# Kernel optimization log

Measured on AMD Instinct MI355X. Metric: run time of the kernel, lower is better.

Reference implementation:

```python
import jax, jax.numpy as jnp
import numpy as np

EPS = 1e-6


def softmax_kernel_transformation(data, is_query, projection_matrix):
    # data: [B,L,H,D], projection_matrix: [M,D]
    d = data.shape[-1]
    m = projection_matrix.shape[0]
    data_normalizer = 1.0 / jnp.sqrt(jnp.sqrt(jnp.float32(d)))
    data = data_normalizer * data
    ratio = 1.0 / jnp.sqrt(jnp.float32(m))
    data_dash = jnp.einsum('blhd,md->blhm', data, projection_matrix)
    diag_data = jnp.sum(jnp.square(data), axis=-1, keepdims=True) / 2.0  # [B,L,H,1]
    if is_query:
        stab = jnp.max(data_dash, axis=-1, keepdims=True)  # per-position max over M
    else:
        stab = jnp.max(data_dash, axis=(1, 3), keepdims=True)  # max over L and M
    return ratio * (jnp.exp(data_dash - diag_data - stab) + EPS)


def causal_linear_attention(qp, kp, v):
    # qp,kp: [L,B,H,M]; v: [L,B,H,D]. Sequential prefix-sum recurrence (FAVOR+ causal).
    B, H, M = qp.shape[1], qp.shape[2], qp.shape[3]
    D = v.shape[-1]
    kv0 = jnp.zeros((B, H, M, D), dtype=v.dtype)
    ks0 = jnp.zeros((B, H, M), dtype=kp.dtype)

    def step(carry, inp):
        kv_sum, k_sum = carry
        q_t, k_t, v_t = inp  # [B,H,M], [B,H,M], [B,H,D]
        kv_sum = kv_sum + jnp.einsum('bhm,bhd->bhmd', k_t, v_t)
        k_sum = k_sum + k_t
        num_t = jnp.einsum('bhmd,bhm->bhd', kv_sum, q_t)  # numerator row
        den_t = jnp.einsum('bhm,bhm->bh', q_t, k_sum)     # normalizer row
        return (kv_sum, k_sum), (num_t, den_t)

    (_, _), (num, den) = jax.lax.scan(step, (kv0, ks0), (qp, kp, v))
    return num, den  # [L,B,H,D], [L,B,H]


def favor_attention(query, key, value, projection_matrix):
    query_prime = softmax_kernel_transformation(query, True, projection_matrix)   # [B,L,H,M]
    key_prime = softmax_kernel_transformation(key, False, projection_matrix)      # [B,L,H,M]
    qp = jnp.transpose(query_prime, (1, 0, 2, 3))  # [L,B,H,M]
    kp = jnp.transpose(key_prime, (1, 0, 2, 3))
    v = jnp.transpose(value, (1, 0, 2, 3))         # [L,B,H,D]
    num, den = causal_linear_attention(qp, kp, v)
    av = jnp.transpose(num, (1, 0, 2, 3))          # [B,L,H,D]
    norm = jnp.transpose(den, (1, 0, 2))[..., None]  # [B,L,H,1]
    return av / norm


def setup_inputs() -> dict:
    B, L, H, D, M = 2, 2048, 8, 64, 128
    root = jax.random.key(0)
    kq, kk, kv, kp = jax.random.split(root, 4)
    return {
        'query': jax.random.normal(kq, (B, L, H, D), dtype=jnp.float32),
        'key': jax.random.normal(kk, (B, L, H, D), dtype=jnp.float32),
        'value': jax.random.normal(kv, (B, L, H, D), dtype=jnp.float32),
        'projection_matrix': jax.random.normal(kp, (M, D), dtype=jnp.float32),
    }


def reference(query, key, value, projection_matrix):
    return favor_attention(query, key, value, projection_matrix)
```

## Files before the change

kernel.cpp:

```cpp
#include <hip/hip_runtime.h>
#include <math.h>

typedef __attribute__((ext_vector_type(8))) short short8;
typedef __attribute__((ext_vector_type(4))) float f32x4;
typedef __attribute__((ext_vector_type(4))) unsigned short u16x4;

constexpr int B_ = 2, L_ = 2048, H_ = 8, D_ = 64, M_ = 128;
constexpr int T_ = 64;
constexpr int C_ = L_ / T_;
constexpr float DN_ = 0.35355339059327373f;
constexpr float RATIO_ = 0.08838834764831845f;
constexpr float EPSV_ = 1e-6f;
constexpr float REPS_ = RATIO_ * EPSV_;
constexpr float KEPS_ = 64.0f * REPS_;

__device__ inline unsigned short f2bf(float x) {
  const unsigned u = __float_as_uint(x);
  return (unsigned short)((u + 0x7fffu + ((u >> 16) & 1u)) >> 16);
}
__device__ inline float bf2f(unsigned short h) {
  return __uint_as_float(((unsigned)h) << 16);
}

__global__ __launch_bounds__(256) void psplit_kernel(
    const float* __restrict__ P, unsigned short* __restrict__ Ph,
    unsigned short* __restrict__ Pl) {
  const int i = blockIdx.x * 256 + threadIdx.x;
  const f32x4 t4 = *reinterpret_cast<const f32x4*>(&P[(size_t)i * 4]);
  u16x4 hi, lo;
#pragma unroll
  for (int j = 0; j < 4; ++j) {
    hi[j] = f2bf(t4[j]);
    lo[j] = f2bf(t4[j] - bf2f(hi[j]));
  }
  *reinterpret_cast<u16x4*>(&Ph[(size_t)i * 4]) = hi;
  *reinterpret_cast<u16x4*>(&Pl[(size_t)i * 4]) = lo;
}

__global__ __launch_bounds__(256) void feat_kernel(
    const float* __restrict__ q, const float* __restrict__ k,
    const unsigned short* __restrict__ Ph, const unsigned short* __restrict__ Pl,
    const float* __restrict__ v, unsigned short* __restrict__ qp16,
    unsigned short* __restrict__ kp16, unsigned short* __restrict__ kvc16,
    float* __restrict__ ksc, unsigned short* __restrict__ vt16,
    float* __restrict__ blockmax, float* __restrict__ vsum) {
  __shared__ __align__(16) unsigned short sm[27648];
  __shared__ float diag_s[T_];
  __shared__ float wred_s[2][T_];
  __shared__ float red4_s[4];

  const int sub = blockIdx.x;
  const int c = sub % C_, bh = sub / C_;
  const int b = bh >> 3, h = bh & 7;
  const int tid = threadIdx.x;
  const int w = tid >> 6, lane = tid & 63;
  const int l15 = lane & 15, l16 = lane >> 4;
  const int rblk = (w >> 1) * 32, cblk = (w & 1) * 64;

  for (int i8 = tid; i8 < M_ * 8; i8 += 256) {
    const int m = i8 >> 3, d0 = (i8 & 7) * 8;
    *reinterpret_cast<short8*>(&sm[9216 + m * 72 + d0]) =
        *reinterpret_cast<const short8*>(&Ph[m * D_ + d0]);
    *reinterpret_cast<short8*>(&sm[18432 + m * 72 + d0]) =
        *reinterpret_cast<const short8*>(&Pl[m * D_ + d0]);
  }

#define STAGE_X(xptr)                                                         \
  for (int i4 = tid; i4 < T_ * 16; i4 += 256) {                               \
    const int r = i4 >> 4, d0 = (i4 & 15) * 4;                                \
    f32x4 t4 = *reinterpret_cast<const f32x4*>(                               \
        &(xptr)[((size_t)(b * L_ + c * T_ + r) * H_ + h) * D_ + d0]);         \
    u16x4 hi, lo;                                                             \
    float sq = 0.f;                                                           \
    _Pragma("unroll") for (int j = 0; j < 4; ++j) {                           \
      const float xv = t4[j] * DN_;                                           \
      sq += xv * xv;                                                          \
      const unsigned short hb = f2bf(xv);                                     \
      hi[j] = hb;                                                             \
      lo[j] = f2bf(xv - bf2f(hb));                                            \
    }                                                                         \
    *reinterpret_cast<u16x4*>(&sm[r * 72 + d0]) = hi;                         \
    *reinterpret_cast<u16x4*>(&sm[4608 + r * 72 + d0]) = lo;                  \
    _Pragma("unroll") for (int off = 1; off < 16; off <<= 1)                  \
        sq += __shfl_xor(sq, off, 64);                                        \
    if ((tid & 15) == 0) diag_s[r] = sq;                                      \
  }

#define DASH_MFMA(accv)                                                       \
  _Pragma("unroll") for (int kk = 0; kk < 2; ++kk) {                          \
    short8 ah[2], al[2], bh8[4], bl8[4];                                      \
    _Pragma("unroll") for (int ti = 0; ti < 2; ++ti) {                        \
      ah[ti] = *reinterpret_cast<const short8*>(                              \
          &sm[(rblk + ti * 16 + l15) * 72 + kk * 32 + l16 * 8]);              \
      al[ti] = *reinterpret_cast<const short8*>(                              \
          &sm[4608 + (rblk + ti * 16 + l15) * 72 + kk * 32 + l16 * 8]);       \
    }                                                                         \
    _Pragma("unroll") for (int tj = 0; tj < 4; ++tj) {                        \
      bh8[tj] = *reinterpret_cast<const short8*>(                             \
          &sm[9216 + (cblk + tj * 16 + l15) * 72 + kk * 32 + l16 * 8]);       \
      bl8[tj] = *reinterpret_cast<const short8*>(                             \
          &sm[18432 + (cblk + tj * 16 + l15) * 72 + kk * 32 + l16 * 8]);      \
    }                                                                         \
    _Pragma("unroll") for (int ti = 0; ti < 2; ++ti)                          \
        _Pragma("unroll") for (int tj = 0; tj < 4; ++tj) {                    \
      accv[ti][tj] = __builtin_amdgcn_mfma_f32_16x16x32_bf16(                 \
          al[ti], bh8[tj], accv[ti][tj], 0, 0, 0);                            \
      accv[ti][tj] = __builtin_amdgcn_mfma_f32_16x16x32_bf16(                 \
          ah[ti], bl8[tj], accv[ti][tj], 0, 0, 0);                            \
      accv[ti][tj] = __builtin_amdgcn_mfma_f32_16x16x32_bf16(                 \
          ah[ti], bh8[tj], accv[ti][tj], 0, 0, 0);                            \
    }                                                                         \
  }

  STAGE_X(q);
  __syncthreads();
  f32x4 acc[2][4];
#pragma unroll
  for (int i = 0; i < 2; ++i)
#pragma unroll
    for (int j = 0; j < 4; ++j) acc[i][j] = {0.f, 0.f, 0.f, 0.f};
  DASH_MFMA(acc);

  {
    float rmax[2][4];
#pragma unroll
    for (int ti = 0; ti < 2; ++ti)
#pragma unroll
      for (int j = 0; j < 4; ++j) {
        float m0 = fmaxf(fmaxf(acc[ti][0][j], acc[ti][1][j]),
                         fmaxf(acc[ti][2][j], acc[ti][3][j]));
#pragma unroll
        for (int off = 1; off < 16; off <<= 1)
          m0 = fmaxf(m0, __shfl_xor(m0, off, 64));
        rmax[ti][j] = m0;
      }
    if (l15 == 0) {
#pragma unroll
      for (int ti = 0; ti < 2; ++ti)
#pragma unroll
        for (int j = 0; j < 4; ++j)
          wred_s[w & 1][rblk + ti * 16 + l16 * 4 + j] = rmax[ti][j];
    }
    __syncthreads();
#pragma unroll
    for (int ti = 0; ti < 2; ++ti)
#pragma unroll
      for (int j = 0; j < 4; ++j) {
        const int row = rblk + ti * 16 + l16 * 4 + j;
        const float sub2 =
            0.5f * diag_s[row] + fmaxf(wred_s[0][row], wred_s[1][row]);
#pragma unroll
        for (int tj = 0; tj < 4; ++tj) {
          const int col = cblk + tj * 16 + l15;
          sm[row * 136 + col] =
              f2bf(RATIO_ * (expf(acc[ti][tj][j] - sub2) + EPSV_));
        }
      }
    __syncthreads();
    unsigned short* outr = qp16 + ((size_t)bh * L_ + c * T_) * M_;
    for (int i8 = tid; i8 < T_ * 16; i8 += 256) {
      const int row = i8 >> 4, m0 = (i8 & 15) * 8;
      *reinterpret_cast<short8*>(&outr[row * M_ + m0]) =
          *reinterpret_cast<const short8*>(&sm[row * 136 + m0]);
    }
  }
  __syncthreads();

  STAGE_X(k);
  __syncthreads();
#pragma unroll
  for (int i = 0; i < 2; ++i)
#pragma unroll
    for (int j = 0; j < 4; ++j) acc[i][j] = {0.f, 0.f, 0.f, 0.f};
  DASH_MFMA(acc);

  float bm = -INFINITY;
#pragma unroll
  for (int ti = 0; ti < 2; ++ti)
#pragma unroll
    for (int tj = 0; tj < 4; ++tj)
#pragma unroll
      for (int j = 0; j < 4; ++j) bm = fmaxf(bm, acc[ti][tj][j]);
#pragma unroll
  for (int off = 1; off < 64; off <<= 1) bm = fmaxf(bm, __shfl_xor(bm, off, 64));
  if (lane == 0) red4_s[w] = bm;
  __syncthreads();
  const float lmax =
      fmaxf(fmaxf(red4_s[0], red4_s[1]), fmaxf(red4_s[2], red4_s[3]));
  if (tid == 0) blockmax[sub] = lmax;

  unsigned short* kpr = kp16 + ((size_t)bh * L_ + c * T_) * M_;
#pragma unroll
  for (int ti = 0; ti < 2; ++ti)
#pragma unroll
    for (int j = 0; j < 4; ++j) {
      const int row = rblk + ti * 16 + l16 * 4 + j;
      const float sub2 = 0.5f * diag_s[row] + lmax;
#pragma unroll
      for (int tj = 0; tj < 4; ++tj) {
        const int col = cblk + tj * 16 + l15;
        const unsigned short us = f2bf(RATIO_ * expf(acc[ti][tj][j] - sub2));
        kpr[row * M_ + col] = us;
        sm[9216 + col * 72 + row] = us;
      }
    }
  for (int i = tid; i < T_ * D_; i += 256) {
    const int t = i & 63, d = i >> 6;
    sm[d * 72 + t] =
        f2bf(v[((size_t)(b * L_ + c * T_ + t) * H_ + h) * D_ + d]);
  }
  __syncthreads();

  unsigned short* vg = vt16 + (size_t)(bh * C_ + c) * (D_ * T_);
  for (int i8 = tid; i8 < D_ * 8; i8 += 256) {
    const int d = i8 >> 3, t0 = (i8 & 7) * 8;
    *reinterpret_cast<short8*>(&vg[d * T_ + t0]) =
        *reinterpret_cast<const short8*>(&sm[d * 72 + t0]);
  }
  if (tid < M_) {
    float s = 0.f;
#pragma unroll
    for (int t8 = 0; t8 < 8; ++t8) {
      const short8 h8 =
          *reinterpret_cast<const short8*>(&sm[9216 + tid * 72 + t8 * 8]);
#pragma unroll
      for (int j = 0; j < 8; ++j) s += bf2f((unsigned short)h8[j]);
    }
    ksc[(size_t)(bh * C_ + c) * M_ + tid] = s;
  }
  if (tid >= 128 && tid < 128 + D_) {
    const int d = tid - 128;
    float s = 0.f;
#pragma unroll
    for (int t8 = 0; t8 < 8; ++t8) {
      const short8 h8 = *reinterpret_cast<const short8*>(&sm[d * 72 + t8 * 8]);
#pragma unroll
      for (int j = 0; j < 8; ++j) s += bf2f((unsigned short)h8[j]);
    }
    vsum[(size_t)(bh * C_ + c) * D_ + d] = s;
  }
  f32x4 acc2[2][4];
#pragma unroll
  for (int i = 0; i < 2; ++i)
#pragma unroll
    for (int j = 0; j < 4; ++j) acc2[i][j] = {0.f, 0.f, 0.f, 0.f};
#pragma unroll
  for (int kk = 0; kk < 2; ++kk) {
    short8 av[2], bv[4];
#pragma unroll
    for (int ti = 0; ti < 2; ++ti)
      av[ti] = *reinterpret_cast<const short8*>(
          &sm[(rblk + ti * 16 + l15) * 72 + kk * 32 + l16 * 8]);
#pragma unroll
    for (int tj = 0; tj < 4; ++tj)
      bv[tj] = *reinterpret_cast<const short8*>(
          &sm[9216 + (cblk + tj * 16 + l15) * 72 + kk * 32 + l16 * 8]);
#pragma unroll
    for (int ti = 0; ti < 2; ++ti)
#pragma unroll
      for (int tj = 0; tj < 4; ++tj)
        acc2[ti][tj] = __builtin_amdgcn_mfma_f32_16x16x32_bf16(
            av[ti], bv[tj], acc2[ti][tj], 0, 0, 0);
  }
#pragma unroll
  for (int ti = 0; ti < 2; ++ti)
#pragma unroll
    for (int j = 0; j < 4; ++j) {
      const int row = rblk + ti * 16 + l16 * 4 + j;
#pragma unroll
      for (int tj = 0; tj < 4; ++tj) {
        const int col = cblk + tj * 16 + l15;
        sm[18432 + row * 136 + col] = f2bf(acc2[ti][tj][j]);
      }
    }
  __syncthreads();
  unsigned short* ob = kvc16 + (size_t)(bh * C_ + c) * (M_ * D_);
  for (int i8 = tid; i8 < D_ * 16; i8 += 256) {
    const int d = i8 >> 4, m0 = (i8 & 15) * 8;
    *reinterpret_cast<short8*>(&ob[d * M_ + m0]) =
        *reinterpret_cast<const short8*>(&sm[18432 + d * 136 + m0]);
  }
#undef STAGE_X
#undef DASH_MFMA
}

__global__ __launch_bounds__(256) void prefix_kernel(
    const unsigned short* __restrict__ kvc16,
    unsigned short* __restrict__ kvp16, float* __restrict__ ksc,
    const float* __restrict__ blockmax, const float* __restrict__ vsum) {
  __shared__ float bm_s[C_];
  __shared__ float sc_s[C_];
  __shared__ float vs_s[2][C_];
  const int bid = blockIdx.x;
  const int ej = bid & 31, bh = bid >> 5;
  if (threadIdx.x < C_) bm_s[threadIdx.x] = blockmax[bh * C_ + threadIdx.x];
  if (threadIdx.x >= 64 && threadIdx.x < 64 + 2 * C_) {
    const int t = threadIdx.x - 64;
    const int ld = t >> 5, cc = t & 31;
    vs_s[ld][cc] = vsum[(size_t)(bh * C_ + cc) * D_ + ej * 2 + ld];
  }
  __syncthreads();
  if (threadIdx.x < C_) {
    float km = -INFINITY;
#pragma unroll
    for (int cc = 0; cc < C_; ++cc) km = fmaxf(km, bm_s[cc]);
    sc_s[threadIdx.x] = expf(bm_s[threadIdx.x] - km);
  }
  __syncthreads();
  const int e = ej * 256 + threadIdx.x;
  const int dl = threadIdx.x >> 7;
  float vals[C_];
#pragma unroll
  for (int cc = 0; cc < C_; ++cc)
    vals[cc] = bf2f(kvc16[(size_t)(bh * C_ + cc) * (M_ * D_) + e]) * sc_s[cc] +
               REPS_ * vs_s[dl][cc];
  float run = 0.f;
#pragma unroll
  for (int cc = 0; cc < C_; ++cc) {
    const float t = vals[cc];
    vals[cc] = run;
    run += t;
  }
#pragma unroll
  for (int cc = 0; cc < C_; ++cc)
    kvp16[(size_t)(bh * C_ + cc) * (M_ * D_) + e] = f2bf(vals[cc]);
  if (ej == 0 && threadIdx.x < M_) {
    const int m = threadIdx.x;
    float ks[C_];
#pragma unroll
    for (int cc = 0; cc < C_; ++cc)
      ks[cc] = ksc[(size_t)(bh * C_ + cc) * M_ + m] * sc_s[cc] + KEPS_;
    float rs = 0.f;
#pragma unroll
    for (int cc = 0; cc < C_; ++cc) {
      const float t = ks[cc];
      ks[cc] = rs;
      rs += t;
    }
#pragma unroll
    for (int cc = 0; cc < C_; ++cc)
      ksc[(size_t)(bh * C_ + cc) * M_ + m] = ks[cc];
  }
}

__global__ __launch_bounds__(256, 3) void intra_kernel(
    const unsigned short* __restrict__ qp16,
    const unsigned short* __restrict__ kp16,
    const unsigned short* __restrict__ vt16,
    const unsigned short* __restrict__ kvp16, const float* __restrict__ ksp,
    const float* __restrict__ blockmax, float* __restrict__ out) {
  __shared__ __align__(16) unsigned short qp_s[T_][136];
  __shared__ __align__(16) unsigned short kp_s[T_][136];
  __shared__ __align__(16) unsigned short S_s[T_][72];
  __shared__ float ksp_s[M_];
  __shared__ float denp_s[4][T_];
  __shared__ float den_s[T_];
  __shared__ float qsum_s[T_];
  __shared__ float bm_s[C_];

  const int bid = blockIdx.x;
  const int c = bid % C_, bh = bid / C_;
  const int b = bh >> 3, h = bh & 7;
  const int tid = threadIdx.x;
  const int w = tid >> 6, lane = tid & 63;
  const int l15 = lane & 15, l16 = lane >> 4;

  const unsigned short* qpt = qp16 + ((size_t)bh * L_ + c * T_) * M_;
  const unsigned short* kpt = kp16 + ((size_t)bh * L_ + c * T_) * M_;
  const unsigned short* kvt = kvp16 + (size_t)(bh * C_ + c) * (M_ * D_);
  const unsigned short* vg = vt16 + (size_t)(bh * C_ + c) * (D_ * T_);

  if (tid < C_) bm_s[tid] = blockmax[bh * C_ + tid];
  for (int i8 = tid; i8 < T_ * 16; i8 += 256) {
    const int r = i8 >> 4, m0 = (i8 & 15) * 8;
    *reinterpret_cast<short8*>(&qp_s[r][m0]) =
        *reinterpret_cast<const short8*>(&qpt[r * M_ + m0]);
    *reinterpret_cast<short8*>(&kp_s[r][m0]) =
        *reinterpret_cast<const short8*>(&kpt[r * M_ + m0]);
  }
  if (tid < M_) ksp_s[tid] = ksp[(size_t)(bh * C_ + c) * M_ + tid];
  __syncthreads();

  {
    const int row = w * 16 + (lane >> 2), mseg = (lane & 3) * 32;
    float p = 0.f;
#pragma unroll
    for (int u = 0; u < 4; ++u) {
      const short8 h8 =
          *reinterpret_cast<const short8*>(&qp_s[row][mseg + u * 8]);
#pragma unroll
      for (int j = 0; j < 8; ++j) p += bf2f((unsigned short)h8[j]);
    }
    p += __shfl_xor(p, 1, 64);
    p += __shfl_xor(p, 2, 64);
    if ((lane & 3) == 0) qsum_s[row] = p;
  }
  __syncthreads();

  float km = -INFINITY;
#pragma unroll
  for (int cc = 0; cc < C_; ++cc) km = fmaxf(km, bm_s[cc]);
  const float sc = expf(bm_s[c] - km);

  const int rblk = (w >> 1) * 32, cblk = (w & 1) * 32;
  f32x4 Sacc[2][2];
#pragma unroll
  for (int i = 0; i < 2; ++i)
#pragma unroll
    for (int j = 0; j < 2; ++j) Sacc[i][j] = {0.f, 0.f, 0.f, 0.f};

#pragma unroll
  for (int kk = 0; kk < 4; ++kk) {
    short8 af[2], bf[2];
#pragma unroll
    for (int ti = 0; ti < 2; ++ti)
      af[ti] = *reinterpret_cast<const short8*>(
          &qp_s[rblk + ti * 16 + l15][kk * 32 + l16 * 8]);
#pragma unroll
    for (int tj = 0; tj < 2; ++tj)
      bf[tj] = *reinterpret_cast<const short8*>(
          &kp_s[cblk + tj * 16 + l15][kk * 32 + l16 * 8]);
#pragma unroll
    for (int ti = 0; ti < 2; ++ti)
#pragma unroll
      for (int tj = 0; tj < 2; ++tj)
        Sacc[ti][tj] = __builtin_amdgcn_mfma_f32_16x16x32_bf16(
            af[ti], bf[tj], Sacc[ti][tj], 0, 0, 0);
  }
#pragma unroll
  for (int ti = 0; ti < 2; ++ti)
#pragma unroll
    for (int tj = 0; tj < 2; ++tj)
#pragma unroll
      for (int j = 0; j < 4; ++j) {
        const int row = rblk + ti * 16 + l16 * 4 + j;
        const int col = cblk + tj * 16 + l15;
        const float add = REPS_ * qsum_s[row];
        const float sv = (col <= row) ? Sacc[ti][tj][j] * sc + add : 0.f;
        S_s[row][col] = f2bf(sv);
      }
  __syncthreads();

  {
    const int t = lane;
    float p = 0.f;
    if (w == 0) {
      for (int tp = 0; tp < 32; ++tp) p += bf2f(S_s[t][tp]);
    } else if (w == 1) {
      for (int tp = 32; tp < 64; ++tp) p += bf2f(S_s[t][tp]);
    } else if (w == 2) {
      for (int m = 0; m < 64; ++m) p += bf2f(qp_s[t][m]) * ksp_s[m];
    } else {
      for (int m = 64; m < 128; ++m) p += bf2f(qp_s[t][m]) * ksp_s[m];
    }
    denp_s[w][t] = p;
  }
  __syncthreads();
  if (tid < T_)
    den_s[tid] =
        denp_s[0][tid] + denp_s[1][tid] + denp_s[2][tid] + denp_s[3][tid];
  __syncthreads();

  const int dblk = (w & 1) * 32;
  f32x4 Nacc[2][2];
#pragma unroll
  for (int i = 0; i < 2; ++i)
#pragma unroll
    for (int j = 0; j < 2; ++j) Nacc[i][j] = {0.f, 0.f, 0.f, 0.f};

#pragma unroll
  for (int kk = 0; kk < 2; ++kk) {
    short8 af[2], bf[2];
#pragma unroll
    for (int ti = 0; ti < 2; ++ti)
      af[ti] = *reinterpret_cast<const short8*>(
          &S_s[rblk + ti * 16 + l15][kk * 32 + l16 * 8]);
#pragma unroll
    for (int tj = 0; tj < 2; ++tj)
      bf[tj] = *reinterpret_cast<const short8*>(
          &vg[(dblk + tj * 16 + l15) * T_ + kk * 32 + l16 * 8]);
#pragma unroll
    for (int ti = 0; ti < 2; ++ti)
#pragma unroll
      for (int tj = 0; tj < 2; ++tj)
        Nacc[ti][tj] = __builtin_amdgcn_mfma_f32_16x16x32_bf16(
            af[ti], bf[tj], Nacc[ti][tj], 0, 0, 0);
  }
#pragma unroll
  for (int kk = 0; kk < 4; ++kk) {
    short8 af[2], bf[2];
#pragma unroll
    for (int ti = 0; ti < 2; ++ti)
      af[ti] = *reinterpret_cast<const short8*>(
          &qp_s[rblk + ti * 16 + l15][kk * 32 + l16 * 8]);
#pragma unroll
    for (int tj = 0; tj < 2; ++tj)
      bf[tj] = *reinterpret_cast<const short8*>(
          &kvt[(dblk + tj * 16 + l15) * M_ + kk * 32 + l16 * 8]);
#pragma unroll
    for (int ti = 0; ti < 2; ++ti)
#pragma unroll
      for (int tj = 0; tj < 2; ++tj)
        Nacc[ti][tj] = __builtin_amdgcn_mfma_f32_16x16x32_bf16(
            af[ti], bf[tj], Nacc[ti][tj], 0, 0, 0);
  }

#pragma unroll
  for (int ti = 0; ti < 2; ++ti)
#pragma unroll
    for (int j = 0; j < 4; ++j) {
      const int row = rblk + ti * 16 + l16 * 4 + j;
      const float r = 1.f / den_s[row];
      float* orow = out + ((size_t)(b * L_ + c * T_ + row) * H_ + h) * D_;
#pragma unroll
      for (int tj = 0; tj < 2; ++tj) {
        const int col = dblk + tj * 16 + l15;
        orow[col] = Nacc[ti][tj][j] * r;
      }
    }
}

extern "C" void kernel_launch(void* const* d_in, const int* in_sizes, int n_in,
                              void* d_out, int out_size, void* d_ws,
                              size_t ws_size, hipStream_t stream) {
  const float* q = (const float*)d_in[0];
  const float* k = (const float*)d_in[1];
  const float* v = (const float*)d_in[2];
  const float* P = (const float*)d_in[3];
  float* out = (float*)d_out;

  float* ws = (float*)d_ws;
  float* blockmax = ws;
  float* ksp = blockmax + 512;
  float* vsum = ksp + (size_t)B_ * H_ * C_ * M_;
  unsigned short* Ph16 = (unsigned short*)(vsum + (size_t)B_ * H_ * C_ * D_);
  unsigned short* Pl16 = Ph16 + M_ * D_;
  unsigned short* qp16 = Pl16 + M_ * D_;
  unsigned short* kp16 = qp16 + (size_t)B_ * H_ * L_ * M_;
  unsigned short* kvc16 = kp16 + (size_t)B_ * H_ * L_ * M_;
  unsigned short* kvp16 = kvc16 + (size_t)B_ * H_ * C_ * D_ * M_;
  unsigned short* vt16 = kvp16 + (size_t)B_ * H_ * C_ * D_ * M_;

  psplit_kernel<<<M_ * D_ / 1024, 256, 0, stream>>>(P, Ph16, Pl16);
  feat_kernel<<<B_ * H_ * C_, 256, 0, stream>>>(q, k, Ph16, Pl16, v, qp16,
                                                kp16, kvc16, ksp, vt16,
                                                blockmax, vsum);
  prefix_kernel<<<B_ * H_ * 32, 256, 0, stream>>>(kvc16, kvp16, ksp, blockmax,
                                                  vsum);
  intra_kernel<<<B_ * H_ * C_, 256, 0, stream>>>(qp16, kp16, vt16, kvp16, ksp,
                                                 blockmax, out);
}
```

Measured before the change: 48.64 us.

## Move intra-chunk QK^T score computation into feature kernel, drop kp16 round trip

The feature kernel now computes the masked intra-chunk score tile Q'K'^T using the key features still in shared memory, along with per-row score sums and query feature sums, and writes a 64x64 bf16 tile to global memory instead of the full key feature matrix. The intra kernel no longer loads key features or runs the score MFMA. It rebuilds the scaled, epsilon-corrected scores on the fly from the stored tile and takes the denominator from the precomputed row sums. This cuts global traffic and frees shared memory so the intra kernel's occupancy hint goes from 3 to 4. The cost is more work and another global read of qp16 inside the feature kernel, plus a closed-form epsilon term in the denominator that could differ slightly from the previous bf16-rounded row sums.

```diff
diff --git a/kernel.cpp b/kernel.cpp
--- a/kernel.cpp
+++ b/kernel.cpp
@@ -41,12 +41,14 @@
     const float* __restrict__ q, const float* __restrict__ k,
     const unsigned short* __restrict__ Ph, const unsigned short* __restrict__ Pl,
     const float* __restrict__ v, unsigned short* __restrict__ qp16,
-    unsigned short* __restrict__ kp16, unsigned short* __restrict__ kvc16,
-    float* __restrict__ ksc, unsigned short* __restrict__ vt16,
-    float* __restrict__ blockmax, float* __restrict__ vsum) {
+    unsigned short* __restrict__ kvc16, float* __restrict__ ksc,
+    unsigned short* __restrict__ vt16, float* __restrict__ blockmax,
+    float* __restrict__ vsum, unsigned short* __restrict__ se_g,
+    float* __restrict__ rsum_g, float* __restrict__ qsum_g) {
   __shared__ __align__(16) unsigned short sm[27648];
   __shared__ float diag_s[T_];
   __shared__ float wred_s[2][T_];
+  __shared__ float qs2_s[2][T_];
   __shared__ float red4_s[4];
 
   const int sub = blockIdx.x;
@@ -149,12 +151,17 @@
         const int row = rblk + ti * 16 + l16 * 4 + j;
         const float sub2 =
             0.5f * diag_s[row] + fmaxf(wred_s[0][row], wred_s[1][row]);
+        float qsp = 0.f;
 #pragma unroll
         for (int tj = 0; tj < 4; ++tj) {
           const int col = cblk + tj * 16 + l15;
-          sm[row * 136 + col] =
-              f2bf(RATIO_ * (expf(acc[ti][tj][j] - sub2) + EPSV_));
+          const float qv = RATIO_ * (expf(acc[ti][tj][j] - sub2) + EPSV_);
+          qsp += qv;
+          sm[row * 136 + col] = f2bf(qv);
         }
+#pragma unroll
+        for (int off = 1; off < 16; off <<= 1) qsp += __shfl_xor(qsp, off, 64);
+        if (l15 == 0) qs2_s[w & 1][row] = qsp;
       }
     __syncthreads();
     unsigned short* outr = qp16 + ((size_t)bh * L_ + c * T_) * M_;
@@ -163,6 +170,8 @@
       *reinterpret_cast<short8*>(&outr[row * M_ + m0]) =
           *reinterpret_cast<const short8*>(&sm[row * 136 + m0]);
     }
+    if (tid < T_)
+      qsum_g[(size_t)(bh * C_ + c) * T_ + tid] = qs2_s[0][tid] + qs2_s[1][tid];
   }
   __syncthreads();
 
@@ -189,7 +198,6 @@
       fmaxf(fmaxf(red4_s[0], red4_s[1]), fmaxf(red4_s[2], red4_s[3]));
   if (tid == 0) blockmax[sub] = lmax;
 
-  unsigned short* kpr = kp16 + ((size_t)bh * L_ + c * T_) * M_;
 #pragma unroll
   for (int ti = 0; ti < 2; ++ti)
 #pragma unroll
@@ -200,8 +208,8 @@
       for (int tj = 0; tj < 4; ++tj) {
         const int col = cblk + tj * 16 + l15;
         const unsigned short us = f2bf(RATIO_ * expf(acc[ti][tj][j] - sub2));
-        kpr[row * M_ + col] = us;
         sm[9216 + col * 72 + row] = us;
+        sm[18432 + row * 136 + col] = us;
       }
     }
   for (int i = tid; i < T_ * D_; i += 256) {
@@ -239,6 +247,7 @@
     }
     vsum[(size_t)(bh * C_ + c) * D_ + d] = s;
   }
+
   f32x4 acc2[2][4];
 #pragma unroll
   for (int i = 0; i < 2; ++i)
@@ -262,6 +271,51 @@
         acc2[ti][tj] = __builtin_amdgcn_mfma_f32_16x16x32_bf16(
             av[ti], bv[tj], acc2[ti][tj], 0, 0, 0);
   }
+
+  const int rs_ = (w >> 1) * 32, cs_ = (w & 1) * 32;
+  const unsigned short* qpt = qp16 + ((size_t)bh * L_ + c * T_) * M_;
+  f32x4 Sacc[2][2];
+#pragma unroll
+  for (int i = 0; i < 2; ++i)
+#pragma unroll
+    for (int j = 0; j < 2; ++j) Sacc[i][j] = {0.f, 0.f, 0.f, 0.f};
+#pragma unroll
+  for (int kk = 0; kk < 4; ++kk) {
+    short8 af[2], bf[2];
+#pragma unroll
+    for (int ti = 0; ti < 2; ++ti)
+      af[ti] = *reinterpret_cast<const short8*>(
+          &qpt[(rs_ + ti * 16 + l15) * M_ + kk * 32 + l16 * 8]);
+#pragma unroll
+    for (int tj = 0; tj < 2; ++tj)
+      bf[tj] = *reinterpret_cast<const short8*>(
+          &sm[18432 + (cs_ + tj * 16 + l15) * 136 + kk * 32 + l16 * 8]);
+#pragma unroll
+    for (int ti = 0; ti < 2; ++ti)
+#pragma unroll
+      for (int tj = 0; tj < 2; ++tj)
+        Sacc[ti][tj] = __builtin_amdgcn_mfma_f32_16x16x32_bf16(
+            af[ti], bf[tj], Sacc[ti][tj], 0, 0, 0);
+  }
+  __syncthreads();
+
+#pragma unroll
+  for (int ti = 0; ti < 2; ++ti)
+#pragma unroll
+    for (int j = 0; j < 4; ++j) {
+      const int row = rs_ + ti * 16 + l16 * 4 + j;
+      float rsp = 0.f;
+#pragma unroll
+      for (int tj = 0; tj < 2; ++tj) {
+        const int col = cs_ + tj * 16 + l15;
+        const float sv = (col <= row) ? Sacc[ti][tj][j] : 0.f;
+        rsp += sv;
+        sm[row * 72 + col] = f2bf(sv);
+      }
+#pragma unroll
+      for (int off = 1; off < 16; off <<= 1) rsp += __shfl_xor(rsp, off, 64);
+      if (l15 == 0) wred_s[w & 1][row] = rsp;
+    }
 #pragma unroll
   for (int ti = 0; ti < 2; ++ti)
 #pragma unroll
@@ -280,6 +334,14 @@
     *reinterpret_cast<short8*>(&ob[d * M_ + m0]) =
         *reinterpret_cast<const short8*>(&sm[18432 + d * 136 + m0]);
   }
+  unsigned short* seo = se_g + (size_t)(bh * C_ + c) * (T_ * T_);
+  for (int i8 = tid; i8 < T_ * 8; i8 += 256) {
+    const int row = i8 >> 3, c0 = (i8 & 7) * 8;
+    *reinterpret_cast<short8*>(&seo[row * T_ + c0]) =
+        *reinterpret_cast<const short8*>(&sm[row * 72 + c0]);
+  }
+  if (tid < T_)
+    rsum_g[(size_t)(bh * C_ + c) * T_ + tid] = wred_s[0][tid] + wred_s[1][tid];
 #undef STAGE_X
 #undef DASH_MFMA
 }
@@ -343,19 +405,18 @@
   }
 }
 
-__global__ __launch_bounds__(256, 3) void intra_kernel(
+__global__ __launch_bounds__(256, 4) void intra_kernel(
     const unsigned short* __restrict__ qp16,
-    const unsigned short* __restrict__ kp16,
-    const unsigned short* __restrict__ vt16,
+    const unsigned short* __restrict__ se_g, const float* __restrict__ rsum_g,
+    const float* __restrict__ qsum_g, const unsigned short* __restrict__ vt16,
     const unsigned short* __restrict__ kvp16, const float* __restrict__ ksp,
     const float* __restrict__ blockmax, float* __restrict__ out) {
   __shared__ __align__(16) unsigned short qp_s[T_][136];
-  __shared__ __align__(16) unsigned short kp_s[T_][136];
-  __shared__ __align__(16) unsigned short S_s[T_][72];
   __shared__ float ksp_s[M_];
   __shared__ float denp_s[4][T_];
   __shared__ float den_s[T_];
   __shared__ float qsum_s[T_];
+  __shared__ float rsum_s[T_];
   __shared__ float bm_s[C_];
 
   const int bid = blockIdx.x;
@@ -366,7 +427,7 @@
   const int l15 = lane & 15, l16 = lane >> 4;
 
   const unsigned short* qpt = qp16 + ((size_t)bh * L_ + c * T_) * M_;
-  const unsigned short* kpt = kp16 + ((size_t)bh * L_ + c * T_) * M_;
+  const unsigned short* seg = se_g + (size_t)(bh * C_ + c) * (T_ * T_);
   const unsigned short* kvt = kvp16 + (size_t)(bh * C_ + c) * (M_ * D_);
   const unsigned short* vg = vt16 + (size_t)(bh * C_ + c) * (D_ * T_);
 
@@ -375,93 +436,33 @@
     const int r = i8 >> 4, m0 = (i8 & 15) * 8;
     *reinterpret_cast<short8*>(&qp_s[r][m0]) =
         *reinterpret_cast<const short8*>(&qpt[r * M_ + m0]);
-    *reinterpret_cast<short8*>(&kp_s[r][m0]) =
-        *reinterpret_cast<const short8*>(&kpt[r * M_ + m0]);
   }
   if (tid < M_) ksp_s[tid] = ksp[(size_t)(bh * C_ + c) * M_ + tid];
-  __syncthreads();
-
-  {
-    const int row = w * 16 + (lane >> 2), mseg = (lane & 3) * 32;
-    float p = 0.f;
-#pragma unroll
-    for (int u = 0; u < 4; ++u) {
-      const short8 h8 =
-          *reinterpret_cast<const short8*>(&qp_s[row][mseg + u * 8]);
-#pragma unroll
-      for (int j = 0; j < 8; ++j) p += bf2f((unsigned short)h8[j]);
-    }
-    p += __shfl_xor(p, 1, 64);
-    p += __shfl_xor(p, 2, 64);
-    if ((lane & 3) == 0) qsum_s[row] = p;
-  }
+  if (tid >= 128 && tid < 128 + T_)
+    qsum_s[tid - 128] = qsum_g[(size_t)(bh * C_ + c) * T_ + tid - 128];
+  if (tid >= 192)
+    rsum_s[tid - 192] = rsum_g[(size_t)(bh * C_ + c) * T_ + tid - 192];
   __syncthreads();
 
   float km = -INFINITY;
 #pragma unroll
   for (int cc = 0; cc < C_; ++cc) km = fmaxf(km, bm_s[cc]);
   const float sc = expf(bm_s[c] - km);
-
-  const int rblk = (w >> 1) * 32, cblk = (w & 1) * 32;
-  f32x4 Sacc[2][2];
-#pragma unroll
-  for (int i = 0; i < 2; ++i)
-#pragma unroll
-    for (int j = 0; j < 2; ++j) Sacc[i][j] = {0.f, 0.f, 0.f, 0.f};
-
-#pragma unroll
-  for (int kk = 0; kk < 4; ++kk) {
-    short8 af[2], bf[2];
-#pragma unroll
-    for (int ti = 0; ti < 2; ++ti)
-      af[ti] = *reinterpret_cast<const short8*>(
-          &qp_s[rblk + ti * 16 + l15][kk * 32 + l16 * 8]);
-#pragma unroll
-    for (int tj = 0; tj < 2; ++tj)
-      bf[tj] = *reinterpret_cast<const short8*>(
-          &kp_s[cblk + tj * 16 + l15][kk * 32 + l16 * 8]);
-#pragma unroll
-    for (int ti = 0; ti < 2; ++ti)
-#pragma unroll
-      for (int tj = 0; tj < 2; ++tj)
-        Sacc[ti][tj] = __builtin_amdgcn_mfma_f32_16x16x32_bf16(
-            af[ti], bf[tj], Sacc[ti][tj], 0, 0, 0);
-  }
-#pragma unroll
-  for (int ti = 0; ti < 2; ++ti)
-#pragma unroll
-    for (int tj = 0; tj < 2; ++tj)
-#pragma unroll
-      for (int j = 0; j < 4; ++j) {
-        const int row = rblk + ti * 16 + l16 * 4 + j;
-        const int col = cblk + tj * 16 + l15;
-        const float add = REPS_ * qsum_s[row];
-        const float sv = (col <= row) ? Sacc[ti][tj][j] * sc + add : 0.f;
-        S_s[row][col] = f2bf(sv);
-      }
-  __syncthreads();
 
   {
     const int t = lane;
     float p = 0.f;
-    if (w == 0) {
-      for (int tp = 0; tp < 32; ++tp) p += bf2f(S_s[t][tp]);
-    } else if (w == 1) {
-      for (int tp = 32; tp < 64; ++tp) p += bf2f(S_s[t][tp]);
-    } else if (w == 2) {
-      for (int m = 0; m < 64; ++m) p += bf2f(qp_s[t][m]) * ksp_s[m];
-    } else {
-      for (int m = 64; m < 128; ++m) p += bf2f(qp_s[t][m]) * ksp_s[m];
-    }
+    for (int m = w * 32; m < w * 32 + 32; ++m) p += bf2f(qp_s[t][m]) * ksp_s[m];
     denp_s[w][t] = p;
   }
   __syncthreads();
   if (tid < T_)
-    den_s[tid] =
-        denp_s[0][tid] + denp_s[1][tid] + denp_s[2][tid] + denp_s[3][tid];
-  __syncthreads();
-
-  const int dblk = (w & 1) * 32;
+    den_s[tid] = denp_s[0][tid] + denp_s[1][tid] + denp_s[2][tid] +
+                 denp_s[3][tid] + sc * rsum_s[tid] +
+                 REPS_ * qsum_s[tid] * (float)(tid + 1);
+  __syncthreads();
+
+  const int rblk = (w >> 1) * 32, dblk = (w & 1) * 32;
   f32x4 Nacc[2][2];
 #pragma unroll
   for (int i = 0; i < 2; ++i)
@@ -472,9 +473,21 @@
   for (int kk = 0; kk < 2; ++kk) {
     short8 af[2], bf[2];
 #pragma unroll
-    for (int ti = 0; ti < 2; ++ti)
-      af[ti] = *reinterpret_cast<const short8*>(
-          &S_s[rblk + ti * 16 + l15][kk * 32 + l16 * 8]);
+    for (int ti = 0; ti < 2; ++ti) {
+      const int row = rblk + ti * 16 + l15;
+      const short8 s8 = *reinterpret_cast<const short8*>(
+          &seg[row * T_ + kk * 32 + l16 * 8]);
+      const float add = REPS_ * qsum_s[row];
+      short8 o;
+#pragma unroll
+      for (int e = 0; e < 8; ++e) {
+        const int col = kk * 32 + l16 * 8 + e;
+        const float fv =
+            (col <= row) ? sc * bf2f((unsigned short)s8[e]) + add : 0.f;
+        o[e] = (short)f2bf(fv);
+      }
+      af[ti] = o;
+    }
 #pragma unroll
     for (int tj = 0; tj < 2; ++tj)
       bf[tj] = *reinterpret_cast<const short8*>(
@@ -533,20 +546,22 @@
   float* blockmax = ws;
   float* ksp = blockmax + 512;
   float* vsum = ksp + (size_t)B_ * H_ * C_ * M_;
-  unsigned short* Ph16 = (unsigned short*)(vsum + (size_t)B_ * H_ * C_ * D_);
+  float* rsum = vsum + (size_t)B_ * H_ * C_ * D_;
+  float* qsum = rsum + (size_t)B_ * H_ * C_ * T_;
+  unsigned short* Ph16 = (unsigned short*)(qsum + (size_t)B_ * H_ * C_ * T_);
   unsigned short* Pl16 = Ph16 + M_ * D_;
   unsigned short* qp16 = Pl16 + M_ * D_;
-  unsigned short* kp16 = qp16 + (size_t)B_ * H_ * L_ * M_;
-  unsigned short* kvc16 = kp16 + (size_t)B_ * H_ * L_ * M_;
+  unsigned short* kvc16 = qp16 + (size_t)B_ * H_ * L_ * M_;
   unsigned short* kvp16 = kvc16 + (size_t)B_ * H_ * C_ * D_ * M_;
   unsigned short* vt16 = kvp16 + (size_t)B_ * H_ * C_ * D_ * M_;
+  unsigned short* se16 = vt16 + (size_t)B_ * H_ * C_ * D_ * T_;
 
   psplit_kernel<<<M_ * D_ / 1024, 256, 0, stream>>>(P, Ph16, Pl16);
   feat_kernel<<<B_ * H_ * C_, 256, 0, stream>>>(q, k, Ph16, Pl16, v, qp16,
-                                                kp16, kvc16, ksp, vt16,
-                                                blockmax, vsum);
+                                                kvc16, ksp, vt16, blockmax,
+                                                vsum, se16, rsum, qsum);
   prefix_kernel<<<B_ * H_ * 32, 256, 0, stream>>>(kvc16, kvp16, ksp, blockmax,
                                                   vsum);
-  intra_kernel<<<B_ * H_ * C_, 256, 0, stream>>>(qp16, kp16, vt16, kvp16, ksp,
-                                                 blockmax, out);
-}
+  intra_kernel<<<B_ * H_ * C_, 256, 0, stream>>>(qp16, se16, rsum, qsum, vt16,
+                                                 kvp16, ksp, blockmax, out);
+}
```

New measurement: 50.44 us. +3.7%, slower.

## Fuse projection split into feature kernel and prefetch K/V and intra operands

Applied to the files above, without the earlier changes.

Removes the separate psplit kernel launch; each feature block now converts the fp32 projection matrix to bf16 hi/lo pairs itself. K and V tiles are loaded into registers at kernel start so their global latency overlaps the Q-side work, and the V transpose is done from registers instead of strided scalar global reads. The intra kernel preloads its V and KV-prefix MFMA operands into registers before the main computation, and feat_kernel gets a two-blocks-per-CU launch bound. The cost is redundant P conversion in every block and higher register pressure.

```diff
diff --git a/kernel.cpp b/kernel.cpp
--- a/kernel.cpp
+++ b/kernel.cpp
@@ -22,28 +22,13 @@
   return __uint_as_float(((unsigned)h) << 16);
 }
 
-__global__ __launch_bounds__(256) void psplit_kernel(
-    const float* __restrict__ P, unsigned short* __restrict__ Ph,
-    unsigned short* __restrict__ Pl) {
-  const int i = blockIdx.x * 256 + threadIdx.x;
-  const f32x4 t4 = *reinterpret_cast<const f32x4*>(&P[(size_t)i * 4]);
-  u16x4 hi, lo;
-#pragma unroll
-  for (int j = 0; j < 4; ++j) {
-    hi[j] = f2bf(t4[j]);
-    lo[j] = f2bf(t4[j] - bf2f(hi[j]));
-  }
-  *reinterpret_cast<u16x4*>(&Ph[(size_t)i * 4]) = hi;
-  *reinterpret_cast<u16x4*>(&Pl[(size_t)i * 4]) = lo;
-}
-
-__global__ __launch_bounds__(256) void feat_kernel(
+__global__ __launch_bounds__(256, 2) void feat_kernel(
     const float* __restrict__ q, const float* __restrict__ k,
-    const unsigned short* __restrict__ Ph, const unsigned short* __restrict__ Pl,
-    const float* __restrict__ v, unsigned short* __restrict__ qp16,
-    unsigned short* __restrict__ kp16, unsigned short* __restrict__ kvc16,
-    float* __restrict__ ksc, unsigned short* __restrict__ vt16,
-    float* __restrict__ blockmax, float* __restrict__ vsum) {
+    const float* __restrict__ P, const float* __restrict__ v,
+    unsigned short* __restrict__ qp16, unsigned short* __restrict__ kp16,
+    unsigned short* __restrict__ kvc16, float* __restrict__ ksc,
+    unsigned short* __restrict__ vt16, float* __restrict__ blockmax,
+    float* __restrict__ vsum) {
   __shared__ __align__(16) unsigned short sm[27648];
   __shared__ float diag_s[T_];
   __shared__ float wred_s[2][T_];
@@ -57,33 +42,48 @@
   const int l15 = lane & 15, l16 = lane >> 4;
   const int rblk = (w >> 1) * 32, cblk = (w & 1) * 64;
 
-  for (int i8 = tid; i8 < M_ * 8; i8 += 256) {
-    const int m = i8 >> 3, d0 = (i8 & 7) * 8;
-    *reinterpret_cast<short8*>(&sm[9216 + m * 72 + d0]) =
-        *reinterpret_cast<const short8*>(&Ph[m * D_ + d0]);
-    *reinterpret_cast<short8*>(&sm[18432 + m * 72 + d0]) =
-        *reinterpret_cast<const short8*>(&Pl[m * D_ + d0]);
-  }
-
-#define STAGE_X(xptr)                                                         \
-  for (int i4 = tid; i4 < T_ * 16; i4 += 256) {                               \
-    const int r = i4 >> 4, d0 = (i4 & 15) * 4;                                \
-    f32x4 t4 = *reinterpret_cast<const f32x4*>(                               \
-        &(xptr)[((size_t)(b * L_ + c * T_ + r) * H_ + h) * D_ + d0]);         \
-    u16x4 hi, lo;                                                             \
-    float sq = 0.f;                                                           \
-    _Pragma("unroll") for (int j = 0; j < 4; ++j) {                           \
-      const float xv = t4[j] * DN_;                                           \
-      sq += xv * xv;                                                          \
-      const unsigned short hb = f2bf(xv);                                     \
-      hi[j] = hb;                                                             \
-      lo[j] = f2bf(xv - bf2f(hb));                                            \
-    }                                                                         \
-    *reinterpret_cast<u16x4*>(&sm[r * 72 + d0]) = hi;                         \
-    *reinterpret_cast<u16x4*>(&sm[4608 + r * 72 + d0]) = lo;                  \
-    _Pragma("unroll") for (int off = 1; off < 16; off <<= 1)                  \
-        sq += __shfl_xor(sq, off, 64);                                        \
-    if ((tid & 15) == 0) diag_s[r] = sq;                                      \
+  f32x4 kreg[4], vreg[4];
+#pragma unroll
+  for (int it = 0; it < 4; ++it) {
+    const int i4 = tid + 256 * it;
+    const int r = i4 >> 4, d0 = (i4 & 15) * 4;
+    kreg[it] = *reinterpret_cast<const f32x4*>(
+        &k[((size_t)(b * L_ + c * T_ + r) * H_ + h) * D_ + d0]);
+    vreg[it] = *reinterpret_cast<const f32x4*>(
+        &v[((size_t)(b * L_ + c * T_ + r) * H_ + h) * D_ + d0]);
+  }
+
+  for (int i4 = tid; i4 < M_ * 16; i4 += 256) {
+    const int m = i4 >> 4, d0 = (i4 & 15) * 4;
+    const f32x4 t4 = *reinterpret_cast<const f32x4*>(&P[m * D_ + d0]);
+    u16x4 hi, lo;
+#pragma unroll
+    for (int j = 0; j < 4; ++j) {
+      hi[j] = f2bf(t4[j]);
+      lo[j] = f2bf(t4[j] - bf2f(hi[j]));
+    }
+    *reinterpret_cast<u16x4*>(&sm[9216 + m * 72 + d0]) = hi;
+    *reinterpret_cast<u16x4*>(&sm[18432 + m * 72 + d0]) = lo;
+  }
+  for (int i4 = tid; i4 < T_ * 16; i4 += 256) {
+    const int r = i4 >> 4, d0 = (i4 & 15) * 4;
+    f32x4 t4 = *reinterpret_cast<const f32x4*>(
+        &q[((size_t)(b * L_ + c * T_ + r) * H_ + h) * D_ + d0]);
+    u16x4 hi, lo;
+    float sq = 0.f;
+#pragma unroll
+    for (int j = 0; j < 4; ++j) {
+      const float xv = t4[j] * DN_;
+      sq += xv * xv;
+      const unsigned short hb = f2bf(xv);
+      hi[j] = hb;
+      lo[j] = f2bf(xv - bf2f(hb));
+    }
+    *reinterpret_cast<u16x4*>(&sm[r * 72 + d0]) = hi;
+    *reinterpret_cast<u16x4*>(&sm[4608 + r * 72 + d0]) = lo;
+#pragma unroll
+    for (int off = 1; off < 16; off <<= 1) sq += __shfl_xor(sq, off, 64);
+    if ((tid & 15) == 0) diag_s[r] = sq;
   }
 
 #define DASH_MFMA(accv)                                                       \
@@ -112,7 +112,6 @@
     }                                                                         \
   }
 
-  STAGE_X(q);
   __syncthreads();
   f32x4 acc[2][4];
 #pragma unroll
@@ -166,7 +165,26 @@
   }
   __syncthreads();
 
-  STAGE_X(k);
+#pragma unroll
+  for (int it = 0; it < 4; ++it) {
+    const int i4 = tid + 256 * it;
+    const int r = i4 >> 4, d0 = (i4 & 15) * 4;
+    u16x4 hi, lo;
+    float sq = 0.f;
+#pragma unroll
+    for (int j = 0; j < 4; ++j) {
+      const float xv = kreg[it][j] * DN_;
+      sq += xv * xv;
+      const unsigned short hb = f2bf(xv);
+      hi[j] = hb;
+      lo[j] = f2bf(xv - bf2f(hb));
+    }
+    *reinterpret_cast<u16x4*>(&sm[r * 72 + d0]) = hi;
+    *reinterpret_cast<u16x4*>(&sm[4608 + r * 72 + d0]) = lo;
+#pragma unroll
+    for (int off = 1; off < 16; off <<= 1) sq += __shfl_xor(sq, off, 64);
+    if ((tid & 15) == 0) diag_s[r] = sq;
+  }
   __syncthreads();
 #pragma unroll
   for (int i = 0; i < 2; ++i)
@@ -204,10 +222,12 @@
         sm[9216 + col * 72 + row] = us;
       }
     }
-  for (int i = tid; i < T_ * D_; i += 256) {
-    const int t = i & 63, d = i >> 6;
-    sm[d * 72 + t] =
-        f2bf(v[((size_t)(b * L_ + c * T_ + t) * H_ + h) * D_ + d]);
+#pragma unroll
+  for (int it = 0; it < 4; ++it) {
+    const int i4 = tid + 256 * it;
+    const int t = i4 >> 4, d0 = (i4 & 15) * 4;
+#pragma unroll
+    for (int j = 0; j < 4; ++j) sm[(d0 + j) * 72 + t] = f2bf(vreg[it][j]);
   }
   __syncthreads();
 
@@ -280,7 +300,6 @@
     *reinterpret_cast<short8*>(&ob[d * M_ + m0]) =
         *reinterpret_cast<const short8*>(&sm[18432 + d * 136 + m0]);
   }
-#undef STAGE_X
 #undef DASH_MFMA
 }
 
@@ -364,11 +383,26 @@
   const int tid = threadIdx.x;
   const int w = tid >> 6, lane = tid & 63;
   const int l15 = lane & 15, l16 = lane >> 4;
+  const int dblk = (w & 1) * 32;
 
   const unsigned short* qpt = qp16 + ((size_t)bh * L_ + c * T_) * M_;
   const unsigned short* kpt = kp16 + ((size_t)bh * L_ + c * T_) * M_;
   const unsigned short* kvt = kvp16 + (size_t)(bh * C_ + c) * (M_ * D_);
   const unsigned short* vg = vt16 + (size_t)(bh * C_ + c) * (D_ * T_);
+
+  short8 vtr[2][2], kvr[4][2];
+#pragma unroll
+  for (int kk = 0; kk < 2; ++kk)
+#pragma unroll
+    for (int tj = 0; tj < 2; ++tj)
+      vtr[kk][tj] = *reinterpret_cast<const short8*>(
+          &vg[(dblk + tj * 16 + l15) * T_ + kk * 32 + l16 * 8]);
+#pragma unroll
+  for (int kk = 0; kk < 4; ++kk)
+#pragma unroll
+    for (int tj = 0; tj < 2; ++tj)
+      kvr[kk][tj] = *reinterpret_cast<const short8*>(
+          &kvt[(dblk + tj * 16 + l15) * M_ + kk * 32 + l16 * 8]);
 
   if (tid < C_) bm_s[tid] = blockmax[bh * C_ + tid];
   for (int i8 = tid; i8 < T_ * 16; i8 += 256) {
@@ -461,7 +495,6 @@
         denp_s[0][tid] + denp_s[1][tid] + denp_s[2][tid] + denp_s[3][tid];
   __syncthreads();
 
-  const int dblk = (w & 1) * 32;
   f32x4 Nacc[2][2];
 #pragma unroll
   for (int i = 0; i < 2; ++i)
@@ -470,39 +503,31 @@
 
 #pragma unroll
   for (int kk = 0; kk < 2; ++kk) {
-    short8 af[2], bf[2];
+    short8 af[2];
 #pragma unroll
     for (int ti = 0; ti < 2; ++ti)
       af[ti] = *reinterpret_cast<const short8*>(
           &S_s[rblk + ti * 16 + l15][kk * 32 + l16 * 8]);
 #pragma unroll
-    for (int tj = 0; tj < 2; ++tj)
-      bf[tj] = *reinterpret_cast<const short8*>(
-          &vg[(dblk + tj * 16 + l15) * T_ + kk * 32 + l16 * 8]);
-#pragma unroll
     for (int ti = 0; ti < 2; ++ti)
 #pragma unroll
       for (int tj = 0; tj < 2; ++tj)
         Nacc[ti][tj] = __builtin_amdgcn_mfma_f32_16x16x32_bf16(
-            af[ti], bf[tj], Nacc[ti][tj], 0, 0, 0);
+            af[ti], vtr[kk][tj], Nacc[ti][tj], 0, 0, 0);
   }
 #pragma unroll
   for (int kk = 0; kk < 4; ++kk) {
-    short8 af[2], bf[2];
+    short8 af[2];
 #pragma unroll
     for (int ti = 0; ti < 2; ++ti)
       af[ti] = *reinterpret_cast<const short8*>(
           &qp_s[rblk + ti * 16 + l15][kk * 32 + l16 * 8]);
 #pragma unroll
-    for (int tj = 0; tj < 2; ++tj)
-      bf[tj] = *reinterpret_cast<const short8*>(
-          &kvt[(dblk + tj * 16 + l15) * M_ + kk * 32 + l16 * 8]);
-#pragma unroll
     for (int ti = 0; ti < 2; ++ti)
 #pragma unroll
       for (int tj = 0; tj < 2; ++tj)
         Nacc[ti][tj] = __builtin_amdgcn_mfma_f32_16x16x32_bf16(
-            af[ti], bf[tj], Nacc[ti][tj], 0, 0, 0);
+            af[ti], kvr[kk][tj], Nacc[ti][tj], 0, 0, 0);
   }
 
 #pragma unroll
@@ -533,18 +558,14 @@
   float* blockmax = ws;
   float* ksp = blockmax + 512;
   float* vsum = ksp + (size_t)B_ * H_ * C_ * M_;
-  unsigned short* Ph16 = (unsigned short*)(vsum + (size_t)B_ * H_ * C_ * D_);
-  unsigned short* Pl16 = Ph16 + M_ * D_;
-  unsigned short* qp16 = Pl16 + M_ * D_;
+  unsigned short* qp16 = (unsigned short*)(vsum + (size_t)B_ * H_ * C_ * D_);
   unsigned short* kp16 = qp16 + (size_t)B_ * H_ * L_ * M_;
   unsigned short* kvc16 = kp16 + (size_t)B_ * H_ * L_ * M_;
   unsigned short* kvp16 = kvc16 + (size_t)B_ * H_ * C_ * D_ * M_;
   unsigned short* vt16 = kvp16 + (size_t)B_ * H_ * C_ * D_ * M_;
 
-  psplit_kernel<<<M_ * D_ / 1024, 256, 0, stream>>>(P, Ph16, Pl16);
-  feat_kernel<<<B_ * H_ * C_, 256, 0, stream>>>(q, k, Ph16, Pl16, v, qp16,
-                                                kp16, kvc16, ksp, vt16,
-                                                blockmax, vsum);
+  feat_kernel<<<B_ * H_ * C_, 256, 0, stream>>>(q, k, P, v, qp16, kp16, kvc16,
+                                                ksp, vt16, blockmax, vsum);
   prefix_kernel<<<B_ * H_ * 32, 256, 0, stream>>>(kvc16, kvp16, ksp, blockmax,
                                                   vsum);
   intra_kernel<<<B_ * H_ * C_, 256, 0, stream>>>(qp16, kp16, vt16, kvp16, ksp,
```

New measurement: 44.49 us. 8.5% less time.
